# Kernel optimization log

Measured on AMD Instinct MI355X. Metric: run time of the kernel, lower is better.

## Reference

```python
import jax, jax.numpy as jnp
import numpy as np

TAU = 2.0
TH = 1.0


def setup_inputs() -> dict:
    key = jax.random.key(0)
    x = jax.random.normal(key, (32, 512, 2048), dtype=jnp.float32)  # [B, T, D]
    return {"x": x}


def reference(x):
    # Leaky-integrate-and-fire recurrence over time axis T.
    # v_t = v_{t-1} + (x_t - v_{t-1}) / tau
    # s_t = sigmoid(v_t - th)          (surrogate spike, used as forward output here)
    # v_t = v_t * (1 - s_t)            (soft multiplicative reset)
    B, T, D = x.shape
    xt = jnp.swapaxes(x, 0, 1)  # [T, B, D] for scan

    def step(v, x_t):
        v = v + (x_t - v) / TAU
        s = jax.nn.sigmoid(v - TH)
        v = v * (1.0 - s)
        return v, s

    v0 = jnp.zeros((B, D), dtype=x.dtype)
    _, spikes = jax.lax.scan(step, v0, xt)  # spikes: [T, B, D]
    return jnp.swapaxes(spikes, 0, 1)  # [B, T, D]
```

## Files before the change

### kernel.cpp

```cpp
#include <hip/hip_runtime.h>
#include <math.h>


#define TAU_INV 0.5f
#define TH 1.0f

constexpr int BATCH = 32;
constexpr int TT = 512;
constexpr int DD = 2048;
constexpr int U = 16;
constexpr int NB = TT / U;

__global__ __launch_bounds__(256) void lif_kernel(const float* __restrict__ x,
                                                  float* __restrict__ out) {
    int tid = blockIdx.x * blockDim.x + threadIdx.x;
    int b = tid >> 11;
    int d = tid & (DD - 1);
    const float* xp = x + (size_t)b * TT * DD + d;
    float* op = out + (size_t)b * TT * DD + d;

    float buf[2][U];

    #pragma unroll
    for (int i = 0; i < U; ++i)
        buf[0][i] = __builtin_nontemporal_load(xp + (size_t)i * DD);

    float v = 0.0f;
    #pragma unroll 2
    for (int blk = 0; blk < NB; ++blk) {
        const int cur = blk & 1;
        const int nxt = cur ^ 1;

        if (blk + 1 < NB) {
            const float* xn = xp + (size_t)(blk + 1) * U * DD;
            #pragma unroll
            for (int i = 0; i < U; ++i)
                buf[nxt][i] = __builtin_nontemporal_load(xn + (size_t)i * DD);
        }

        float* ob = op + (size_t)blk * U * DD;
        #pragma unroll
        for (int i = 0; i < U; ++i) {
            v = v + (buf[cur][i] - v) * TAU_INV;
            float s = 1.0f / (1.0f + __expf(TH - v));
            __builtin_nontemporal_store(s, ob + (size_t)i * DD);
            v = v * (1.0f - s);
        }
    }
}

extern "C" void kernel_launch(void* const* d_in, const int* in_sizes, int n_in,
                              void* d_out, int out_size, void* d_ws, size_t ws_size,
                              hipStream_t stream) {
    const float* x = (const float*)d_in[0];
    float* out = (float*)d_out;
    const int threads = 256;
    const int total = BATCH * DD;
    const int blocks = (total + threads - 1) / threads;
    lif_kernel<<<blocks, threads, 0, stream>>>(x, out);
}
```

Measured before the change: 226.8 us.

## Split time axis into segments with warm-up recurrence for more parallelism

Each (batch, feature) recurrence is split into 8 time segments processed by separate threads, giving eight times more threads. Each segment after the first starts from zero state and replays a 16-step warm-up, relying on the fact that each step multiplies the memory of the initial state by at most 0.5. The goal is to fill the GPU, which previously ran only 256 blocks each stuck on a 512-step serial chain. The cost is 25% extra input reads plus a small truncation error, and nontemporal loads are replaced with ordinary loads.

```diff
diff --git a/kernel.cpp b/kernel.cpp
--- a/kernel.cpp
+++ b/kernel.cpp
@@ -8,37 +8,59 @@
 constexpr int BATCH = 32;
 constexpr int TT = 512;
 constexpr int DD = 2048;
-constexpr int U = 16;
-constexpr int NB = TT / U;
+constexpr int SEG = 8;
+constexpr int SEGLEN = TT / SEG;
+constexpr int WARM = 16;
+constexpr int U = 8;
 
-__global__ __launch_bounds__(256) void lif_kernel(const float* __restrict__ x,
-                                                  float* __restrict__ out) {
+__global__ __launch_bounds__(256, 8) void lif_kernel(const float* __restrict__ x,
+                                                     float* __restrict__ out) {
     int tid = blockIdx.x * blockDim.x + threadIdx.x;
-    int b = tid >> 11;
-    int d = tid & (DD - 1);
-    const float* xp = x + (size_t)b * TT * DD + d;
-    float* op = out + (size_t)b * TT * DD + d;
+    int d   = tid & (DD - 1);
+    int b   = (tid >> 11) & (BATCH - 1);
+    int seg = tid >> 16;
+    const size_t base = (size_t)b * TT * DD + d;
+    const float* xp = x + base;
+    float* op = out + base;
+    const int t0 = seg * SEGLEN;
 
+    float v = 0.0f;
+
+    if (seg > 0) {
+        const float* xw = xp + (size_t)(t0 - WARM) * DD;
+        #pragma unroll
+        for (int w0 = 0; w0 < WARM; w0 += U) {
+            float xs[U];
+            #pragma unroll
+            for (int i = 0; i < U; ++i)
+                xs[i] = xw[(size_t)(w0 + i) * DD];
+            #pragma unroll
+            for (int i = 0; i < U; ++i) {
+                v = v + (xs[i] - v) * TAU_INV;
+                float s = 1.0f / (1.0f + __expf(TH - v));
+                v = v * (1.0f - s);
+            }
+        }
+    }
+
+    const float* xm = xp + (size_t)t0 * DD;
+    float* om = op + (size_t)t0 * DD;
     float buf[2][U];
-
     #pragma unroll
     for (int i = 0; i < U; ++i)
-        buf[0][i] = __builtin_nontemporal_load(xp + (size_t)i * DD);
+        buf[0][i] = xm[(size_t)i * DD];
 
-    float v = 0.0f;
-    #pragma unroll 2
+    constexpr int NB = SEGLEN / U;
+    #pragma unroll
     for (int blk = 0; blk < NB; ++blk) {
-        const int cur = blk & 1;
-        const int nxt = cur ^ 1;
-
+        const int cur = blk & 1, nxt = cur ^ 1;
         if (blk + 1 < NB) {
-            const float* xn = xp + (size_t)(blk + 1) * U * DD;
+            const float* xn = xm + (size_t)(blk + 1) * U * DD;
             #pragma unroll
             for (int i = 0; i < U; ++i)
-                buf[nxt][i] = __builtin_nontemporal_load(xn + (size_t)i * DD);
+                buf[nxt][i] = xn[(size_t)i * DD];
         }
-
-        float* ob = op + (size_t)blk * U * DD;
+        float* ob = om + (size_t)blk * U * DD;
         #pragma unroll
         for (int i = 0; i < U; ++i) {
             v = v + (buf[cur][i] - v) * TAU_INV;
@@ -55,7 +77,7 @@
     const float* x = (const float*)d_in[0];
     float* out = (float*)d_out;
     const int threads = 256;
-    const int total = BATCH * DD;
+    const int total = BATCH * DD * SEG;
     const int blocks = (total + threads - 1) / threads;
     lif_kernel<<<blocks, threads, 0, stream>>>(x, out);
 }
```

Result: slower. 236.6 us (+4.3%).
